# Kernel optimization log

Hardware: AMD Instinct MI355X
Metric: run time of the kernel (lower is better)

The kernel has to match this reference:

```python
import jax, jax.numpy as jnp
import numpy as np

WINDOW_SIZE = 11
SIGMA = 1.5
WEIGHTS = np.array([0.0448, 0.2856, 0.3001, 0.2363, 0.1333], dtype=np.float32)
LEVELS = 5


def _gaussian(ws, sigma):
    x = np.arange(ws, dtype=np.float32)
    g = np.exp(-((x - ws // 2) ** 2) / (2.0 * sigma ** 2))
    return g / g.sum()


def _window3d(ws, channel):
    g = _gaussian(ws, SIGMA)
    w3 = np.einsum('i,j,k->ijk', g, g, g).astype(np.float32)  # [ws,ws,ws]
    # OIDHW, depthwise: O=channel, I=1
    return jnp.asarray(np.broadcast_to(w3[None, None], (channel, 1, ws, ws, ws)))


def _conv3d(x, w, channel):
    return jax.lax.conv_general_dilated(
        x, w, window_strides=(1, 1, 1), padding='VALID',
        dimension_numbers=('NCDHW', 'OIDHW', 'NCDHW'),
        feature_group_count=channel)


def _avg_pool3d(x):
    s = jax.lax.reduce_window(x, 0.0, jax.lax.add,
                              (1, 1, 2, 2, 2), (1, 1, 2, 2, 2), 'VALID')
    return s / 8.0


def _ssim(img1, img2, window_size):
    _, channel, d, h, w = img1.shape
    # val_range=None branch: L derived from img1 statistics
    max_val = jnp.where(jnp.max(img1) > 128, 255.0, 1.0)
    min_val = jnp.where(jnp.min(img1) < -0.5, -1.0, 0.0)
    L = max_val - min_val
    real_size = min(window_size, d, h, w)
    win = _window3d(real_size, channel)

    mu1 = _conv3d(img1, win, channel)
    mu2 = _conv3d(img2, win, channel)
    mu1_sq = mu1 * mu1
    mu2_sq = mu2 * mu2
    mu1_mu2 = mu1 * mu2
    sigma1_sq = _conv3d(img1 * img1, win, channel) - mu1_sq
    sigma2_sq = _conv3d(img2 * img2, win, channel) - mu2_sq
    sigma12 = _conv3d(img1 * img2, win, channel) - mu1_mu2

    C1 = (0.01 * L) ** 2
    C2 = (0.03 * L) ** 2
    v1 = 2.0 * sigma12 + C2
    v2 = sigma1_sq + sigma2_sq + C2
    cs = jnp.mean(v1 / v2)
    ssim_map = (2.0 * mu1_mu2 + C1) * v1 / ((mu1_sq + mu2_sq + C1) * v2)
    return jnp.mean(ssim_map), cs


def setup_inputs() -> dict:
    key = jax.random.key(0)
    k1, k2 = jax.random.split(key)
    shape = (2, 1, 192, 192, 192)
    img1 = jax.random.normal(k1, shape, dtype=jnp.float32)
    img2 = jax.random.normal(k2, shape, dtype=jnp.float32)
    return {"img1": img1, "img2": img2}


def reference(img1, img2):
    weights = jnp.asarray(WEIGHTS)
    ssims, mcs = [], []
    for _ in range(LEVELS):
        sim, cs = _ssim(img1, img2, WINDOW_SIZE)
        ssims.append(sim)
        mcs.append(cs)
        img1 = _avg_pool3d(img1)
        img2 = _avg_pool3d(img2)
    ssims = jnp.stack(ssims)
    mcs = jnp.stack(mcs)
    pow1 = mcs ** weights
    pow2 = ssims ** weights
    return jnp.prod(pow1[:-1]) * pow2[-1]
```

## Files before the change

### kernel.cpp

```cpp
#include <hip/hip_runtime.h>
#include <math.h>


__device__ __forceinline__ unsigned enc_f(float f) {
    unsigned u = __float_as_uint(f);
    return (u & 0x80000000u) ? ~u : (u | 0x80000000u);
}
__device__ __forceinline__ float dec_f(unsigned e) {
    unsigned u = (e & 0x80000000u) ? (e ^ 0x80000000u) : ~e;
    return __uint_as_float(u);
}

__global__ void init_kernel(float* wsf) {
    unsigned* wsu = (unsigned*)wsf;
    int t = threadIdx.x;
    if (t < 10)       wsf[t] = 0.0f;
    else if (t < 15)  wsu[t] = 0xFFFFFFFFu;
    else if (t < 20)  wsu[t] = 0u;
    else if (t == 20) wsu[t] = 0u;
}

struct PyrParams {
    const float* src[2];
    float* dst[2][4];
};

__launch_bounds__(256, 4)
__global__ void pyramid_kernel(PyrParams P, float* wsf) {
    __shared__ float L1[16 * 256];
    __shared__ float L2[512];
    __shared__ float L3[64];
    __shared__ float smn[4], smx[4];
    unsigned* wsu = (unsigned*)wsf;

    const int tid = threadIdx.x;
    int blk = blockIdx.x;
    int r = blk % 216; blk /= 216;
    int batch = blk & 1;
    int im = blk >> 1;
    const int rx = r % 6, ry = (r / 6) % 6, rz = r / 36;

    const long N0 = 192L * 192 * 192;
    const float* src = P.src[im] + (long)batch * N0;
    float* d1 = P.dst[im][0] + (long)batch * 96 * 96 * 96;
    float* d2 = P.dst[im][1] + (long)batch * 48 * 48 * 48;
    float* d3 = P.dst[im][2] + (long)batch * 24 * 24 * 24;
    float* d4 = P.dst[im][3] + (long)batch * 12 * 12 * 12;

    const int tx = tid & 15, ty = tid >> 4;
    float mnv[5], mxv[5];
#pragma unroll
    for (int l = 0; l < 5; l++) { mnv[l] = INFINITY; mxv[l] = -INFINITY; }

    const long D = 192, D2 = 192L * 192;
    const int gx = 2 * (rx * 16 + tx);
    const int gy = 2 * (ry * 16 + ty);
#pragma unroll 4
    for (int z = 0; z < 16; z++) {
        const int gz = 2 * (rz * 16 + z);
        long base = (long)gz * D2 + (long)gy * D + gx;
        float2 a00 = *(const float2*)(src + base);
        float2 a01 = *(const float2*)(src + base + D);
        float2 a10 = *(const float2*)(src + base + D2);
        float2 a11 = *(const float2*)(src + base + D2 + D);
        float lo = fminf(fminf(fminf(a00.x, a00.y), fminf(a01.x, a01.y)),
                         fminf(fminf(a10.x, a10.y), fminf(a11.x, a11.y)));
        float hi = fmaxf(fmaxf(fmaxf(a00.x, a00.y), fmaxf(a01.x, a01.y)),
                         fmaxf(fmaxf(a10.x, a10.y), fmaxf(a11.x, a11.y)));
        mnv[0] = fminf(mnv[0], lo); mxv[0] = fmaxf(mxv[0], hi);
        float s = (a00.x + a00.y + a01.x + a01.y +
                   a10.x + a10.y + a11.x + a11.y) * 0.125f;
        mnv[1] = fminf(mnv[1], s); mxv[1] = fmaxf(mxv[1], s);
        d1[(long)(rz * 16 + z) * 96 * 96 + (ry * 16 + ty) * 96 + (rx * 16 + tx)] = s;
        L1[z * 256 + ty * 16 + tx] = s;
    }
    __syncthreads();

#pragma unroll
    for (int k = 0; k < 2; k++) {
        int o = tid + (k << 8);
        int x = o & 7, y = (o >> 3) & 7, z = o >> 6;
        float s = (L1[(2 * z) * 256 + (2 * y) * 16 + 2 * x] +
                   L1[(2 * z) * 256 + (2 * y) * 16 + 2 * x + 1] +
                   L1[(2 * z) * 256 + (2 * y + 1) * 16 + 2 * x] +
                   L1[(2 * z) * 256 + (2 * y + 1) * 16 + 2 * x + 1] +
                   L1[(2 * z + 1) * 256 + (2 * y) * 16 + 2 * x] +
                   L1[(2 * z + 1) * 256 + (2 * y) * 16 + 2 * x + 1] +
                   L1[(2 * z + 1) * 256 + (2 * y + 1) * 16 + 2 * x] +
                   L1[(2 * z + 1) * 256 + (2 * y + 1) * 16 + 2 * x + 1]) * 0.125f;
        mnv[2] = fminf(mnv[2], s); mxv[2] = fmaxf(mxv[2], s);
        d2[(long)(rz * 8 + z) * 48 * 48 + (ry * 8 + y) * 48 + (rx * 8 + x)] = s;
        L2[o] = s;
    }
    __syncthreads();

    if (tid < 64) {
        int x = tid & 3, y = (tid >> 2) & 3, z = tid >> 4;
        float s = (L2[(2 * z) * 64 + (2 * y) * 8 + 2 * x] +
                   L2[(2 * z) * 64 + (2 * y) * 8 + 2 * x + 1] +
                   L2[(2 * z) * 64 + (2 * y + 1) * 8 + 2 * x] +
                   L2[(2 * z) * 64 + (2 * y + 1) * 8 + 2 * x + 1] +
                   L2[(2 * z + 1) * 64 + (2 * y) * 8 + 2 * x] +
                   L2[(2 * z + 1) * 64 + (2 * y) * 8 + 2 * x + 1] +
                   L2[(2 * z + 1) * 64 + (2 * y + 1) * 8 + 2 * x] +
                   L2[(2 * z + 1) * 64 + (2 * y + 1) * 8 + 2 * x + 1]) * 0.125f;
        mnv[3] = fminf(mnv[3], s); mxv[3] = fmaxf(mxv[3], s);
        d3[(long)(rz * 4 + z) * 24 * 24 + (ry * 4 + y) * 24 + (rx * 4 + x)] = s;
        L3[tid] = s;
    }
    __syncthreads();

    if (tid < 8) {
        int x = tid & 1, y = (tid >> 1) & 1, z = tid >> 2;
        float s = (L3[(2 * z) * 16 + (2 * y) * 4 + 2 * x] +
                   L3[(2 * z) * 16 + (2 * y) * 4 + 2 * x + 1] +
                   L3[(2 * z) * 16 + (2 * y + 1) * 4 + 2 * x] +
                   L3[(2 * z) * 16 + (2 * y + 1) * 4 + 2 * x + 1] +
                   L3[(2 * z + 1) * 16 + (2 * y) * 4 + 2 * x] +
                   L3[(2 * z + 1) * 16 + (2 * y) * 4 + 2 * x + 1] +
                   L3[(2 * z + 1) * 16 + (2 * y + 1) * 4 + 2 * x] +
                   L3[(2 * z + 1) * 16 + (2 * y + 1) * 4 + 2 * x + 1]) * 0.125f;
        mnv[4] = fminf(mnv[4], s); mxv[4] = fmaxf(mxv[4], s);
        d4[(long)(rz * 2 + z) * 12 * 12 + (ry * 2 + y) * 12 + (rx * 2 + x)] = s;
    }

    const int lane = tid & 63, w = tid >> 6;
#pragma unroll
    for (int l = 0; l < 5; l++) {
        float mn = mnv[l], mx = mxv[l];
        for (int o = 32; o; o >>= 1) {
            mn = fminf(mn, __shfl_down(mn, o));
            mx = fmaxf(mx, __shfl_down(mx, o));
        }
        __syncthreads();
        if (lane == 0) { smn[w] = mn; smx[w] = mx; }
        __syncthreads();
        if (tid == 0 && im == 0) {
            for (int i = 1; i < 4; i++) { mn = fminf(mn, smn[i]); mx = fmaxf(mx, smx[i]); }
            atomicMin(&wsu[10 + l], enc_f(mn));
            atomicMax(&wsu[15 + l], enc_f(mx));
        }
    }
}

#define TSX 16
#define TSY 32
#define EXR 42
#define EXC 26
#define SPS 30
#define NPIX (EXR * EXC)
#define TPS 17

struct AllParams {
    const float* A[5];
    const float* B[5];
    int D[5], O[5], zc[5], nTx[5], nTy[5];
    int blk0[6];
    float* out;
    double cnt[5];
};

__launch_bounds__(256, 2)
__attribute__((amdgpu_waves_per_eu(2, 2)))
__global__ void ssim_all_kernel(AllParams P, float* wsf) {
    __shared__ __align__(16) float2 S[EXR * SPS];
    __shared__ __align__(16) float4 TX4[EXR * TPS];
    __shared__ float TXe[EXR * TPS];
    __shared__ float2 RED[256];

    const int tid = threadIdx.x;
    const int col = tid & 15;
    const int yg  = tid >> 4;

    int level = 0;
    {
        int b = blockIdx.x;
#pragma unroll
        for (int l = 1; l < 5; l++)
            if (b >= P.blk0[l]) level = l;
    }
    int rel = blockIdx.x - P.blk0[level];
    const int D   = P.D[level];
    const int O   = P.O[level];
    const int ZC  = P.zc[level];
    const int nTx = P.nTx[level];
    const int nTy = P.nTy[level];

    const int tx = rel % nTx;  rel /= nTx;
    const int ty = rel % nTy;  rel /= nTy;
    const int batch = rel & 1;
    const int chunk = rel >> 1;

    const int oz0 = chunk * ZC;
    const int oz1 = min(oz0 + ZC, O);
    const int nplanes = oz1 - oz0 + 10;
    const int ox0 = tx * TSX;
    const int oy0 = ty * TSY;
    const int D2  = D * D;
    const float* A = P.A[level] + (long)batch * D * D2;
    const float* B = P.B[level] + (long)batch * D * D2;

    float g[11];
    {
        float s = 0.f;
#pragma unroll
        for (int i = 0; i < 11; i++) {
            float d = (float)(i - 5);
            g[i] = expf(-d * d / 4.5f);
            s += g[i];
        }
#pragma unroll
        for (int i = 0; i < 11; i++) g[i] /= s;
    }

    const unsigned* wsu = (const unsigned*)wsf;
    float mxv = dec_f(wsu[15 + level]);
    float mnv = dec_f(wsu[10 + level]);
    float maxval = (mxv > 128.f) ? 255.f : 1.f;
    float minval = (mnv < -0.5f) ? -1.f : 0.f;
    float Lr = maxval - minval;
    float C1 = 0.01f * Lr; C1 *= C1;
    float C2 = 0.03f * Lr; C2 *= C2;

    int  poff[5], sidx[5];
    bool pval[5];
#pragma unroll
    for (int k = 0; k < 5; k++) {
        int idx = tid + (k << 8);
        pval[k] = (idx < NPIX);
        int row = idx / EXC;
        int c   = idx - row * EXC;
        sidx[k] = row * SPS + c;
        int gy = min(oy0 + row, D - 1);
        int gx = min(ox0 + c,   D - 1);
        poff[k] = gy * D + gx;
    }

    float Acc[10][11] = {};
    float ssim_acc = 0.f, cs_acc = 0.f;

    const bool vx  = (ox0 + col < O);
    const bool vy0 = vx && (oy0 + 2 * yg < O);
    const bool vy1 = vx && (oy0 + 2 * yg + 1 < O);

    float2 Pld[5];
    {
        long zoff = (long)oz0 * D2;
#pragma unroll
        for (int k = 0; k < 5; k++)
            if (pval[k]) Pld[k] = make_float2(A[zoff + poff[k]], B[zoff + poff[k]]);
    }

    for (int pc = 0; pc < nplanes; ++pc) {
        __syncthreads();
#pragma unroll
        for (int k = 0; k < 5; k++)
            if (pval[k]) S[sidx[k]] = Pld[k];
        if (pc + 1 < nplanes) {
            long zoff = (long)(oz0 + pc + 1) * D2;
#pragma unroll
            for (int k = 0; k < 5; k++)
                if (pval[k]) Pld[k] = make_float2(A[zoff + poff[k]], B[zoff + poff[k]]);
        }
        __syncthreads();

        if (tid < EXR * 4) {
            int row = tid >> 2;
            int cg  = tid & 3;
            const float4* srow = (const float4*)(S + row * SPS);
            float pa[14], pb[14];
#pragma unroll
            for (int i = 0; i < 7; i++) {
                float4 q = srow[2 * cg + i];
                pa[2 * i] = q.x; pb[2 * i] = q.y;
                pa[2 * i + 1] = q.z; pb[2 * i + 1] = q.w;
            }
#pragma unroll
            for (int cc = 0; cc < 4; cc++) {
                float m1 = 0.f, m2 = 0.f, aa = 0.f, bb = 0.f, ab = 0.f;
#pragma unroll
                for (int j = 0; j < 11; j++) {
                    float w = g[j];
                    float a = pa[cc + j], b = pb[cc + j];
                    float wa = w * a, wb = w * b;
                    m1 += wa; m2 += wb;
                    aa += wa * a; bb += wb * b; ab += wa * b;
                }
                int o = row * TPS + 4 * cg + cc;
                TX4[o] = make_float4(m1, m2, aa, bb);
                TXe[o] = ab;
            }
        }
        __syncthreads();

        float se[5] = {0.f, 0.f, 0.f, 0.f, 0.f};
        float so[5] = {0.f, 0.f, 0.f, 0.f, 0.f};
#pragma unroll
        for (int j = 0; j < 12; j++) {
            int o = (2 * yg + j) * TPS + col;
            float4 q = TX4[o];
            float e  = TXe[o];
            if (j < 11) {
                float w = g[j];
                se[0] += w * q.x; se[1] += w * q.y; se[2] += w * q.z;
                se[3] += w * q.w; se[4] += w * e;
            }
            if (j > 0) {
                float w = g[j - 1];
                so[0] += w * q.x; so[1] += w * q.y; so[2] += w * q.z;
                so[3] += w * q.w; so[4] += w * e;
            }
        }

#pragma unroll
        for (int f = 0; f < 5; f++) {
#pragma unroll
            for (int k = 0; k < 10; k++)
                Acc[2 * f][k] = fmaf(g[10 - k], se[f], Acc[2 * f][k + 1]);
            Acc[2 * f][10] = g[0] * se[f];
#pragma unroll
            for (int k = 0; k < 10; k++)
                Acc[2 * f + 1][k] = fmaf(g[10 - k], so[f], Acc[2 * f + 1][k + 1]);
            Acc[2 * f + 1][10] = g[0] * so[f];
        }

        if (pc >= 10) {
#pragma unroll
            for (int r = 0; r < 2; r++) {
                bool valid = r ? vy1 : vy0;
                if (!valid) continue;
                float m1  = Acc[0 + r][0], m2  = Acc[2 + r][0];
                float s11 = Acc[4 + r][0], s22 = Acc[6 + r][0], s12 = Acc[8 + r][0];
                float mu11 = m1 * m1, mu22 = m2 * m2, mu12 = m1 * m2;
                float sg1 = s11 - mu11, sg2 = s22 - mu22, sg12 = s12 - mu12;
                float v1 = 2.f * sg12 + C2;
                float v2 = sg1 + sg2 + C2;
                cs_acc   += v1 / v2;
                ssim_acc += ((2.f * mu12 + C1) * v1) / ((mu11 + mu22 + C1) * v2);
            }
        }
    }

    RED[tid] = make_float2(ssim_acc, cs_acc);
    __syncthreads();
    for (int s = 128; s > 0; s >>= 1) {
        if (tid < s) {
            RED[tid].x += RED[tid + s].x;
            RED[tid].y += RED[tid + s].y;
        }
        __syncthreads();
    }
    if (tid == 0) {
        atomicAdd(&wsf[level],     RED[0].x);
        atomicAdd(&wsf[5 + level], RED[0].y);
        __threadfence();
        unsigned prev = atomicAdd((unsigned*)wsf + 20, 1u);
        if (prev == (unsigned)(P.blk0[5] - 1)) {
            double w[5];
            w[0] = (double)0.0448f; w[1] = (double)0.2856f; w[2] = (double)0.3001f;
            w[3] = (double)0.2363f; w[4] = (double)0.1333f;
            double prod = 1.0;
            for (int l = 0; l < 4; l++) {
                float cs = atomicAdd(&wsf[5 + l], 0.0f);
                prod *= pow((double)cs / P.cnt[l], w[l]);
            }
            float sm = atomicAdd(&wsf[4], 0.0f);
            prod *= pow((double)sm / P.cnt[4], w[4]);
            P.out[0] = (float)prod;
        }
    }
}

extern "C" void kernel_launch(void* const* d_in, const int* in_sizes, int n_in,
                              void* d_out, int out_size, void* d_ws, size_t ws_size,
                              hipStream_t stream) {
    (void)in_sizes; (void)n_in; (void)out_size; (void)ws_size;
    const float* img1 = (const float*)d_in[0];
    const float* img2 = (const float*)d_in[1];
    float* wsf = (float*)d_ws;
    float* out = (float*)d_out;

    const int Ds[5]  = {192, 96, 48, 24, 12};
    const int ZCs[5] = {26, 16, 14, 14, 2};

    float* bufA[5] = {nullptr};
    float* bufB[5] = {nullptr};
    size_t o = 32;
    for (int l = 1; l < 5; l++) {
        long n = 2L * Ds[l] * Ds[l] * Ds[l];
        bufA[l] = wsf + o; o += (size_t)n;
        bufB[l] = wsf + o; o += (size_t)n;
    }

    init_kernel<<<1, 64, 0, stream>>>(wsf);

    PyrParams PP;
    PP.src[0] = img1; PP.src[1] = img2;
    for (int l = 1; l < 5; l++) { PP.dst[0][l - 1] = bufA[l]; PP.dst[1][l - 1] = bufB[l]; }
    pyramid_kernel<<<216 * 2 * 2, 256, 0, stream>>>(PP, wsf);

    AllParams P;
    P.A[0] = img1; P.B[0] = img2;
    for (int l = 1; l < 5; l++) { P.A[l] = bufA[l]; P.B[l] = bufB[l]; }
    P.out = out;
    int acc = 0;
    for (int l = 0; l < 5; l++) {
        int D = Ds[l], O = D - 10, ZC = ZCs[l];
        int nTx = (O + TSX - 1) / TSX;
        int nTy = (O + TSY - 1) / TSY;
        int ZCn = (O + ZC - 1) / ZC;
        P.D[l] = D; P.O[l] = O; P.zc[l] = ZC; P.nTx[l] = nTx; P.nTy[l] = nTy;
        P.blk0[l] = acc;
        acc += nTx * nTy * 2 * ZCn;
        double Od = (double)O;
        P.cnt[l] = 2.0 * Od * Od * Od;
    }
    P.blk0[5] = acc;
    ssim_all_kernel<<<acc, 256, 0, stream>>>(P, wsf);
}
```

Before: 358.6 us.

## Fuse init, pyramid and SSIM into one persistent cooperative kernel

```diff
diff --git a/kernel.cpp b/kernel.cpp
--- a/kernel.cpp
+++ b/kernel.cpp
@@ -1,5 +1,8 @@
 #include <hip/hip_runtime.h>
+#include <hip/hip_cooperative_groups.h>
 #include <math.h>
+
+namespace cg = cooperative_groups;
 
 
 __device__ __forceinline__ unsigned enc_f(float f) {
@@ -11,138 +14,6 @@
     return __uint_as_float(u);
 }
 
-__global__ void init_kernel(float* wsf) {
-    unsigned* wsu = (unsigned*)wsf;
-    int t = threadIdx.x;
-    if (t < 10)       wsf[t] = 0.0f;
-    else if (t < 15)  wsu[t] = 0xFFFFFFFFu;
-    else if (t < 20)  wsu[t] = 0u;
-    else if (t == 20) wsu[t] = 0u;
-}
-
-struct PyrParams {
-    const float* src[2];
-    float* dst[2][4];
-};
-
-__launch_bounds__(256, 4)
-__global__ void pyramid_kernel(PyrParams P, float* wsf) {
-    __shared__ float L1[16 * 256];
-    __shared__ float L2[512];
-    __shared__ float L3[64];
-    __shared__ float smn[4], smx[4];
-    unsigned* wsu = (unsigned*)wsf;
-
-    const int tid = threadIdx.x;
-    int blk = blockIdx.x;
-    int r = blk % 216; blk /= 216;
-    int batch = blk & 1;
-    int im = blk >> 1;
-    const int rx = r % 6, ry = (r / 6) % 6, rz = r / 36;
-
-    const long N0 = 192L * 192 * 192;
-    const float* src = P.src[im] + (long)batch * N0;
-    float* d1 = P.dst[im][0] + (long)batch * 96 * 96 * 96;
-    float* d2 = P.dst[im][1] + (long)batch * 48 * 48 * 48;
-    float* d3 = P.dst[im][2] + (long)batch * 24 * 24 * 24;
-    float* d4 = P.dst[im][3] + (long)batch * 12 * 12 * 12;
-
-    const int tx = tid & 15, ty = tid >> 4;
-    float mnv[5], mxv[5];
-#pragma unroll
-    for (int l = 0; l < 5; l++) { mnv[l] = INFINITY; mxv[l] = -INFINITY; }
-
-    const long D = 192, D2 = 192L * 192;
-    const int gx = 2 * (rx * 16 + tx);
-    const int gy = 2 * (ry * 16 + ty);
-#pragma unroll 4
-    for (int z = 0; z < 16; z++) {
-        const int gz = 2 * (rz * 16 + z);
-        long base = (long)gz * D2 + (long)gy * D + gx;
-        float2 a00 = *(const float2*)(src + base);
-        float2 a01 = *(const float2*)(src + base + D);
-        float2 a10 = *(const float2*)(src + base + D2);
-        float2 a11 = *(const float2*)(src + base + D2 + D);
-        float lo = fminf(fminf(fminf(a00.x, a00.y), fminf(a01.x, a01.y)),
-                         fminf(fminf(a10.x, a10.y), fminf(a11.x, a11.y)));
-        float hi = fmaxf(fmaxf(fmaxf(a00.x, a00.y), fmaxf(a01.x, a01.y)),
-                         fmaxf(fmaxf(a10.x, a10.y), fmaxf(a11.x, a11.y)));
-        mnv[0] = fminf(mnv[0], lo); mxv[0] = fmaxf(mxv[0], hi);
-        float s = (a00.x + a00.y + a01.x + a01.y +
-                   a10.x + a10.y + a11.x + a11.y) * 0.125f;
-        mnv[1] = fminf(mnv[1], s); mxv[1] = fmaxf(mxv[1], s);
-        d1[(long)(rz * 16 + z) * 96 * 96 + (ry * 16 + ty) * 96 + (rx * 16 + tx)] = s;
-        L1[z * 256 + ty * 16 + tx] = s;
-    }
-    __syncthreads();
-
-#pragma unroll
-    for (int k = 0; k < 2; k++) {
-        int o = tid + (k << 8);
-        int x = o & 7, y = (o >> 3) & 7, z = o >> 6;
-        float s = (L1[(2 * z) * 256 + (2 * y) * 16 + 2 * x] +
-                   L1[(2 * z) * 256 + (2 * y) * 16 + 2 * x + 1] +
-                   L1[(2 * z) * 256 + (2 * y + 1) * 16 + 2 * x] +
-                   L1[(2 * z) * 256 + (2 * y + 1) * 16 + 2 * x + 1] +
-                   L1[(2 * z + 1) * 256 + (2 * y) * 16 + 2 * x] +
-                   L1[(2 * z + 1) * 256 + (2 * y) * 16 + 2 * x + 1] +
-                   L1[(2 * z + 1) * 256 + (2 * y + 1) * 16 + 2 * x] +
-                   L1[(2 * z + 1) * 256 + (2 * y + 1) * 16 + 2 * x + 1]) * 0.125f;
-        mnv[2] = fminf(mnv[2], s); mxv[2] = fmaxf(mxv[2], s);
-        d2[(long)(rz * 8 + z) * 48 * 48 + (ry * 8 + y) * 48 + (rx * 8 + x)] = s;
-        L2[o] = s;
-    }
-    __syncthreads();
-
-    if (tid < 64) {
-        int x = tid & 3, y = (tid >> 2) & 3, z = tid >> 4;
-        float s = (L2[(2 * z) * 64 + (2 * y) * 8 + 2 * x] +
-                   L2[(2 * z) * 64 + (2 * y) * 8 + 2 * x + 1] +
-                   L2[(2 * z) * 64 + (2 * y + 1) * 8 + 2 * x] +
-                   L2[(2 * z) * 64 + (2 * y + 1) * 8 + 2 * x + 1] +
-                   L2[(2 * z + 1) * 64 + (2 * y) * 8 + 2 * x] +
-                   L2[(2 * z + 1) * 64 + (2 * y) * 8 + 2 * x + 1] +
-                   L2[(2 * z + 1) * 64 + (2 * y + 1) * 8 + 2 * x] +
-                   L2[(2 * z + 1) * 64 + (2 * y + 1) * 8 + 2 * x + 1]) * 0.125f;
-        mnv[3] = fminf(mnv[3], s); mxv[3] = fmaxf(mxv[3], s);
-        d3[(long)(rz * 4 + z) * 24 * 24 + (ry * 4 + y) * 24 + (rx * 4 + x)] = s;
-        L3[tid] = s;
-    }
-    __syncthreads();
-
-    if (tid < 8) {
-        int x = tid & 1, y = (tid >> 1) & 1, z = tid >> 2;
-        float s = (L3[(2 * z) * 16 + (2 * y) * 4 + 2 * x] +
-                   L3[(2 * z) * 16 + (2 * y) * 4 + 2 * x + 1] +
-                   L3[(2 * z) * 16 + (2 * y + 1) * 4 + 2 * x] +
-                   L3[(2 * z) * 16 + (2 * y + 1) * 4 + 2 * x + 1] +
-                   L3[(2 * z + 1) * 16 + (2 * y) * 4 + 2 * x] +
-                   L3[(2 * z + 1) * 16 + (2 * y) * 4 + 2 * x + 1] +
-                   L3[(2 * z + 1) * 16 + (2 * y + 1) * 4 + 2 * x] +
-                   L3[(2 * z + 1) * 16 + (2 * y + 1) * 4 + 2 * x + 1]) * 0.125f;
-        mnv[4] = fminf(mnv[4], s); mxv[4] = fmaxf(mxv[4], s);
-        d4[(long)(rz * 2 + z) * 12 * 12 + (ry * 2 + y) * 12 + (rx * 2 + x)] = s;
-    }
-
-    const int lane = tid & 63, w = tid >> 6;
-#pragma unroll
-    for (int l = 0; l < 5; l++) {
-        float mn = mnv[l], mx = mxv[l];
-        for (int o = 32; o; o >>= 1) {
-            mn = fminf(mn, __shfl_down(mn, o));
-            mx = fmaxf(mx, __shfl_down(mx, o));
-        }
-        __syncthreads();
-        if (lane == 0) { smn[w] = mn; smx[w] = mx; }
-        __syncthreads();
-        if (tid == 0 && im == 0) {
-            for (int i = 1; i < 4; i++) { mn = fminf(mn, smn[i]); mx = fmaxf(mx, smx[i]); }
-            atomicMin(&wsu[10 + l], enc_f(mn));
-            atomicMax(&wsu[15 + l], enc_f(mx));
-        }
-    }
-}
-
 #define TSX 16
 #define TSY 32
 #define EXR 42
@@ -151,7 +22,9 @@
 #define NPIX (EXR * EXC)
 #define TPS 17
 
-struct AllParams {
+struct MegaParams {
+    const float* src[2];
+    float* dst[2][4];
     const float* A[5];
     const float* B[5];
     int D[5], O[5], zc[5], nTx[5], nTy[5];
@@ -160,45 +33,151 @@
     double cnt[5];
 };
 
+#define LDS_BYTES 26912
+
 __launch_bounds__(256, 2)
 __attribute__((amdgpu_waves_per_eu(2, 2)))
-__global__ void ssim_all_kernel(AllParams P, float* wsf) {
-    __shared__ __align__(16) float2 S[EXR * SPS];
-    __shared__ __align__(16) float4 TX4[EXR * TPS];
-    __shared__ float TXe[EXR * TPS];
-    __shared__ float2 RED[256];
-
+__global__ void mega_kernel(MegaParams P, float* wsf) {
+    __shared__ __align__(16) char LB[LDS_BYTES];
+    __shared__ int sItem;
+    unsigned* wsu = (unsigned*)wsf;
     const int tid = threadIdx.x;
+
+    if (blockIdx.x == 0) {
+        if (tid < 10)       wsf[tid] = 0.0f;
+        else if (tid < 15)  wsu[tid] = 0xFFFFFFFFu;
+        else if (tid < 20)  wsu[tid] = 0u;
+        else if (tid < 22)  wsu[tid] = 0u;
+    }
+    cg::this_grid().sync();
+
+    {
+        float* L1  = (float*)LB;
+        float* L2s = (float*)(LB + 16384);
+        float* L3s = (float*)(LB + 18432);
+        float* smn = (float*)(LB + 18688);
+        float* smx = (float*)(LB + 18704);
+
+        for (int p = blockIdx.x; p < 864; p += gridDim.x) {
+            int blk = p;
+            int r = blk % 216; blk /= 216;
+            int batch = blk & 1;
+            int im = blk >> 1;
+            const int rx = r % 6, ry = (r / 6) % 6, rz = r / 36;
+
+            const long N0 = 192L * 192 * 192;
+            const float* src = P.src[im] + (long)batch * N0;
+            float* d1 = P.dst[im][0] + (long)batch * 96 * 96 * 96;
+            float* d2 = P.dst[im][1] + (long)batch * 48 * 48 * 48;
+            float* d3 = P.dst[im][2] + (long)batch * 24 * 24 * 24;
+            float* d4 = P.dst[im][3] + (long)batch * 12 * 12 * 12;
+
+            const int tx = tid & 15, ty = tid >> 4;
+            float mnv[5], mxv[5];
+#pragma unroll
+            for (int l = 0; l < 5; l++) { mnv[l] = INFINITY; mxv[l] = -INFINITY; }
+
+            const long D = 192, D2 = 192L * 192;
+            const int gx = 2 * (rx * 16 + tx);
+            const int gy = 2 * (ry * 16 + ty);
+#pragma unroll 4
+            for (int z = 0; z < 16; z++) {
+                const int gz = 2 * (rz * 16 + z);
+                long base = (long)gz * D2 + (long)gy * D + gx;
+                float2 a00 = *(const float2*)(src + base);
+                float2 a01 = *(const float2*)(src + base + D);
+                float2 a10 = *(const float2*)(src + base + D2);
+                float2 a11 = *(const float2*)(src + base + D2 + D);
+                float lo = fminf(fminf(fminf(a00.x, a00.y), fminf(a01.x, a01.y)),
+                                 fminf(fminf(a10.x, a10.y), fminf(a11.x, a11.y)));
+                float hi = fmaxf(fmaxf(fmaxf(a00.x, a00.y), fmaxf(a01.x, a01.y)),
+                                 fmaxf(fmaxf(a10.x, a10.y), fmaxf(a11.x, a11.y)));
+                mnv[0] = fminf(mnv[0], lo); mxv[0] = fmaxf(mxv[0], hi);
+                float s = (a00.x + a00.y + a01.x + a01.y +
+                           a10.x + a10.y + a11.x + a11.y) * 0.125f;
+                mnv[1] = fminf(mnv[1], s); mxv[1] = fmaxf(mxv[1], s);
+                d1[(long)(rz * 16 + z) * 96 * 96 + (ry * 16 + ty) * 96 + (rx * 16 + tx)] = s;
+                L1[z * 256 + ty * 16 + tx] = s;
+            }
+            __syncthreads();
+
+#pragma unroll
+            for (int k = 0; k < 2; k++) {
+                int o = tid + (k << 8);
+                int x = o & 7, y = (o >> 3) & 7, z = o >> 6;
+                float s = (L1[(2 * z) * 256 + (2 * y) * 16 + 2 * x] +
+                           L1[(2 * z) * 256 + (2 * y) * 16 + 2 * x + 1] +
+                           L1[(2 * z) * 256 + (2 * y + 1) * 16 + 2 * x] +
+                           L1[(2 * z) * 256 + (2 * y + 1) * 16 + 2 * x + 1] +
+                           L1[(2 * z + 1) * 256 + (2 * y) * 16 + 2 * x] +
+                           L1[(2 * z + 1) * 256 + (2 * y) * 16 + 2 * x + 1] +
+                           L1[(2 * z + 1) * 256 + (2 * y + 1) * 16 + 2 * x] +
+                           L1[(2 * z + 1) * 256 + (2 * y + 1) * 16 + 2 * x + 1]) * 0.125f;
+                mnv[2] = fminf(mnv[2], s); mxv[2] = fmaxf(mxv[2], s);
+                d2[(long)(rz * 8 + z) * 48 * 48 + (ry * 8 + y) * 48 + (rx * 8 + x)] = s;
+                L2s[o] = s;
+            }
+            __syncthreads();
+
+            if (tid < 64) {
+                int x = tid & 3, y = (tid >> 2) & 3, z = tid >> 4;
+                float s = (L2s[(2 * z) * 64 + (2 * y) * 8 + 2 * x] +
+                           L2s[(2 * z) * 64 + (2 * y) * 8 + 2 * x + 1] +
+                           L2s[(2 * z) * 64 + (2 * y + 1) * 8 + 2 * x] +
+                           L2s[(2 * z) * 64 + (2 * y + 1) * 8 + 2 * x + 1] +
+                           L2s[(2 * z + 1) * 64 + (2 * y) * 8 + 2 * x] +
+                           L2s[(2 * z + 1) * 64 + (2 * y) * 8 + 2 * x + 1] +
+                           L2s[(2 * z + 1) * 64 + (2 * y + 1) * 8 + 2 * x] +
+                           L2s[(2 * z + 1) * 64 + (2 * y + 1) * 8 + 2 * x + 1]) * 0.125f;
+                mnv[3] = fminf(mnv[3], s); mxv[3] = fmaxf(mxv[3], s);
+                d3[(long)(rz * 4 + z) * 24 * 24 + (ry * 4 + y) * 24 + (rx * 4 + x)] = s;
+                L3s[tid] = s;
+            }
+            __syncthreads();
+
+            if (tid < 8) {
+                int x = tid & 1, y = (tid >> 1) & 1, z = tid >> 2;
+                float s = (L3s[(2 * z) * 16 + (2 * y) * 4 + 2 * x] +
+                           L3s[(2 * z) * 16 + (2 * y) * 4 + 2 * x + 1] +
+                           L3s[(2 * z) * 16 + (2 * y + 1) * 4 + 2 * x] +
+                           L3s[(2 * z) * 16 + (2 * y + 1) * 4 + 2 * x + 1] +
+                           L3s[(2 * z + 1) * 16 + (2 * y) * 4 + 2 * x] +
+                           L3s[(2 * z + 1) * 16 + (2 * y) * 4 + 2 * x + 1] +
+                           L3s[(2 * z + 1) * 16 + (2 * y + 1) * 4 + 2 * x] +
+                           L3s[(2 * z + 1) * 16 + (2 * y + 1) * 4 + 2 * x + 1]) * 0.125f;
+                mnv[4] = fminf(mnv[4], s); mxv[4] = fmaxf(mxv[4], s);
+                d4[(long)(rz * 2 + z) * 12 * 12 + (ry * 2 + y) * 12 + (rx * 2 + x)] = s;
+            }
+
+            const int lane = tid & 63, w = tid >> 6;
+#pragma unroll
+            for (int l = 0; l < 5; l++) {
+                float mn = mnv[l], mx = mxv[l];
+                for (int o = 32; o; o >>= 1) {
+                    mn = fminf(mn, __shfl_down(mn, o));
+                    mx = fmaxf(mx, __shfl_down(mx, o));
+                }
+                __syncthreads();
+                if (lane == 0) { smn[w] = mn; smx[w] = mx; }
+                __syncthreads();
+                if (tid == 0 && im == 0) {
+                    for (int i = 1; i < 4; i++) { mn = fminf(mn, smn[i]); mx = fmaxf(mx, smx[i]); }
+                    atomicMin(&wsu[10 + l], enc_f(mn));
+                    atomicMax(&wsu[15 + l], enc_f(mx));
+                }
+            }
+            __syncthreads();
+        }
+    }
+    cg::this_grid().sync();
+
+    float2* S   = (float2*)LB;
+    float4* TX4 = (float4*)(LB + 10080);
+    float*  TXe = (float*)(LB + 21504);
+    float2* RED = (float2*)(LB + 24360);
+
     const int col = tid & 15;
     const int yg  = tid >> 4;
-
-    int level = 0;
-    {
-        int b = blockIdx.x;
-#pragma unroll
-        for (int l = 1; l < 5; l++)
-            if (b >= P.blk0[l]) level = l;
-    }
-    int rel = blockIdx.x - P.blk0[level];
-    const int D   = P.D[level];
-    const int O   = P.O[level];
-    const int ZC  = P.zc[level];
-    const int nTx = P.nTx[level];
-    const int nTy = P.nTy[level];
-
-    const int tx = rel % nTx;  rel /= nTx;
-    const int ty = rel % nTy;  rel /= nTy;
-    const int batch = rel & 1;
-    const int chunk = rel >> 1;
-
-    const int oz0 = chunk * ZC;
-    const int oz1 = min(oz0 + ZC, O);
-    const int nplanes = oz1 - oz0 + 10;
-    const int ox0 = tx * TSX;
-    const int oy0 = ty * TSY;
-    const int D2  = D * D;
-    const float* A = P.A[level] + (long)batch * D * D2;
-    const float* B = P.B[level] + (long)batch * D * D2;
 
     float g[11];
     {
@@ -213,160 +192,193 @@
         for (int i = 0; i < 11; i++) g[i] /= s;
     }
 
-    const unsigned* wsu = (const unsigned*)wsf;
-    float mxv = dec_f(wsu[15 + level]);
-    float mnv = dec_f(wsu[10 + level]);
-    float maxval = (mxv > 128.f) ? 255.f : 1.f;
-    float minval = (mnv < -0.5f) ? -1.f : 0.f;
-    float Lr = maxval - minval;
-    float C1 = 0.01f * Lr; C1 *= C1;
-    float C2 = 0.03f * Lr; C2 *= C2;
-
-    int  poff[5], sidx[5];
-    bool pval[5];
-#pragma unroll
-    for (int k = 0; k < 5; k++) {
-        int idx = tid + (k << 8);
-        pval[k] = (idx < NPIX);
-        int row = idx / EXC;
-        int c   = idx - row * EXC;
-        sidx[k] = row * SPS + c;
-        int gy = min(oy0 + row, D - 1);
-        int gx = min(ox0 + c,   D - 1);
-        poff[k] = gy * D + gx;
-    }
-
-    float Acc[10][11] = {};
-    float ssim_acc = 0.f, cs_acc = 0.f;
-
-    const bool vx  = (ox0 + col < O);
-    const bool vy0 = vx && (oy0 + 2 * yg < O);
-    const bool vy1 = vx && (oy0 + 2 * yg + 1 < O);
-
-    float2 Pld[5];
-    {
-        long zoff = (long)oz0 * D2;
-#pragma unroll
-        for (int k = 0; k < 5; k++)
-            if (pval[k]) Pld[k] = make_float2(A[zoff + poff[k]], B[zoff + poff[k]]);
-    }
-
-    for (int pc = 0; pc < nplanes; ++pc) {
+    const int nItems = P.blk0[5];
+
+    for (;;) {
+        if (tid == 0) sItem = (int)atomicAdd(&wsu[21], 1u);
         __syncthreads();
-#pragma unroll
-        for (int k = 0; k < 5; k++)
-            if (pval[k]) S[sidx[k]] = Pld[k];
-        if (pc + 1 < nplanes) {
-            long zoff = (long)(oz0 + pc + 1) * D2;
+        const int item = sItem;
+        if (item >= nItems) break;
+
+        int level = 0;
+#pragma unroll
+        for (int l = 1; l < 5; l++)
+            if (item >= P.blk0[l]) level = l;
+        int rel = item - P.blk0[level];
+        const int D   = P.D[level];
+        const int O   = P.O[level];
+        const int ZC  = P.zc[level];
+        const int nTx = P.nTx[level];
+        const int nTy = P.nTy[level];
+
+        const int tx = rel % nTx;  rel /= nTx;
+        const int ty = rel % nTy;  rel /= nTy;
+        const int batch = rel & 1;
+        const int chunk = rel >> 1;
+
+        const int oz0 = chunk * ZC;
+        const int oz1 = min(oz0 + ZC, O);
+        const int nplanes = oz1 - oz0 + 10;
+        const int ox0 = tx * TSX;
+        const int oy0 = ty * TSY;
+        const int D2  = D * D;
+        const float* A = P.A[level] + (long)batch * D * D2;
+        const float* B = P.B[level] + (long)batch * D * D2;
+
+        float mxv = dec_f(wsu[15 + level]);
+        float mnv = dec_f(wsu[10 + level]);
+        float maxval = (mxv > 128.f) ? 255.f : 1.f;
+        float minval = (mnv < -0.5f) ? -1.f : 0.f;
+        float Lr = maxval - minval;
+        float C1 = 0.01f * Lr; C1 *= C1;
+        float C2 = 0.03f * Lr; C2 *= C2;
+
+        int  poff[5], sidx[5];
+        bool pval[5];
+#pragma unroll
+        for (int k = 0; k < 5; k++) {
+            int idx = tid + (k << 8);
+            pval[k] = (idx < NPIX);
+            int row = idx / EXC;
+            int c   = idx - row * EXC;
+            sidx[k] = row * SPS + c;
+            int gyy = min(oy0 + row, D - 1);
+            int gxx = min(ox0 + c,   D - 1);
+            poff[k] = gyy * D + gxx;
+        }
+
+        float Acc[10][11] = {};
+        float ssim_acc = 0.f, cs_acc = 0.f;
+
+        const bool vx  = (ox0 + col < O);
+        const bool vy0 = vx && (oy0 + 2 * yg < O);
+        const bool vy1 = vx && (oy0 + 2 * yg + 1 < O);
+
+        float2 Pld[5];
+        {
+            long zoff = (long)oz0 * D2;
 #pragma unroll
             for (int k = 0; k < 5; k++)
                 if (pval[k]) Pld[k] = make_float2(A[zoff + poff[k]], B[zoff + poff[k]]);
         }
+
+        for (int pc = 0; pc < nplanes; ++pc) {
+            __syncthreads();
+#pragma unroll
+            for (int k = 0; k < 5; k++)
+                if (pval[k]) S[sidx[k]] = Pld[k];
+            if (pc + 1 < nplanes) {
+                long zoff = (long)(oz0 + pc + 1) * D2;
+#pragma unroll
+                for (int k = 0; k < 5; k++)
+                    if (pval[k]) Pld[k] = make_float2(A[zoff + poff[k]], B[zoff + poff[k]]);
+            }
+            __syncthreads();
+
+            if (tid < EXR * 4) {
+                int row = tid >> 2;
+                int cg2 = tid & 3;
+                const float4* srow = (const float4*)(S + row * SPS);
+                float pa[14], pb[14];
+#pragma unroll
+                for (int i = 0; i < 7; i++) {
+                    float4 q = srow[2 * cg2 + i];
+                    pa[2 * i] = q.x; pb[2 * i] = q.y;
+                    pa[2 * i + 1] = q.z; pb[2 * i + 1] = q.w;
+                }
+#pragma unroll
+                for (int cc = 0; cc < 4; cc++) {
+                    float m1 = 0.f, m2 = 0.f, aa = 0.f, bb = 0.f, ab = 0.f;
+#pragma unroll
+                    for (int j = 0; j < 11; j++) {
+                        float w = g[j];
+                        float a = pa[cc + j], b = pb[cc + j];
+                        float wa = w * a, wb = w * b;
+                        m1 += wa; m2 += wb;
+                        aa += wa * a; bb += wb * b; ab += wa * b;
+                    }
+                    int o = row * TPS + 4 * cg2 + cc;
+                    TX4[o] = make_float4(m1, m2, aa, bb);
+                    TXe[o] = ab;
+                }
+            }
+            __syncthreads();
+
+            float se[5] = {0.f, 0.f, 0.f, 0.f, 0.f};
+            float so[5] = {0.f, 0.f, 0.f, 0.f, 0.f};
+#pragma unroll
+            for (int j = 0; j < 12; j++) {
+                int o = (2 * yg + j) * TPS + col;
+                float4 q = TX4[o];
+                float e  = TXe[o];
+                if (j < 11) {
+                    float w = g[j];
+                    se[0] += w * q.x; se[1] += w * q.y; se[2] += w * q.z;
+                    se[3] += w * q.w; se[4] += w * e;
+                }
+                if (j > 0) {
+                    float w = g[j - 1];
+                    so[0] += w * q.x; so[1] += w * q.y; so[2] += w * q.z;
+                    so[3] += w * q.w; so[4] += w * e;
+                }
+            }
+
+#pragma unroll
+            for (int f = 0; f < 5; f++) {
+#pragma unroll
+                for (int k = 0; k < 10; k++)
+                    Acc[2 * f][k] = fmaf(g[10 - k], se[f], Acc[2 * f][k + 1]);
+                Acc[2 * f][10] = g[0] * se[f];
+#pragma unroll
+                for (int k = 0; k < 10; k++)
+                    Acc[2 * f + 1][k] = fmaf(g[10 - k], so[f], Acc[2 * f + 1][k + 1]);
+                Acc[2 * f + 1][10] = g[0] * so[f];
+            }
+
+            if (pc >= 10) {
+#pragma unroll
+                for (int rr = 0; rr < 2; rr++) {
+                    bool valid = rr ? vy1 : vy0;
+                    if (!valid) continue;
+                    float m1  = Acc[0 + rr][0], m2  = Acc[2 + rr][0];
+                    float s11 = Acc[4 + rr][0], s22 = Acc[6 + rr][0], s12 = Acc[8 + rr][0];
+                    float mu11 = m1 * m1, mu22 = m2 * m2, mu12 = m1 * m2;
+                    float sg1 = s11 - mu11, sg2 = s22 - mu22, sg12 = s12 - mu12;
+                    float v1 = 2.f * sg12 + C2;
+                    float v2 = sg1 + sg2 + C2;
+                    cs_acc   += v1 / v2;
+                    ssim_acc += ((2.f * mu12 + C1) * v1) / ((mu11 + mu22 + C1) * v2);
+                }
+            }
+        }
+
+        RED[tid] = make_float2(ssim_acc, cs_acc);
         __syncthreads();
-
-        if (tid < EXR * 4) {
-            int row = tid >> 2;
-            int cg  = tid & 3;
-            const float4* srow = (const float4*)(S + row * SPS);
-            float pa[14], pb[14];
-#pragma unroll
-            for (int i = 0; i < 7; i++) {
-                float4 q = srow[2 * cg + i];
-                pa[2 * i] = q.x; pb[2 * i] = q.y;
-                pa[2 * i + 1] = q.z; pb[2 * i + 1] = q.w;
-            }
-#pragma unroll
-            for (int cc = 0; cc < 4; cc++) {
-                float m1 = 0.f, m2 = 0.f, aa = 0.f, bb = 0.f, ab = 0.f;
-#pragma unroll
-                for (int j = 0; j < 11; j++) {
-                    float w = g[j];
-                    float a = pa[cc + j], b = pb[cc + j];
-                    float wa = w * a, wb = w * b;
-                    m1 += wa; m2 += wb;
-                    aa += wa * a; bb += wb * b; ab += wa * b;
-                }
-                int o = row * TPS + 4 * cg + cc;
-                TX4[o] = make_float4(m1, m2, aa, bb);
-                TXe[o] = ab;
-            }
-        }
-        __syncthreads();
-
-        float se[5] = {0.f, 0.f, 0.f, 0.f, 0.f};
-        float so[5] = {0.f, 0.f, 0.f, 0.f, 0.f};
-#pragma unroll
-        for (int j = 0; j < 12; j++) {
-            int o = (2 * yg + j) * TPS + col;
-            float4 q = TX4[o];
-            float e  = TXe[o];
-            if (j < 11) {
-                float w = g[j];
-                se[0] += w * q.x; se[1] += w * q.y; se[2] += w * q.z;
-                se[3] += w * q.w; se[4] += w * e;
-            }
-            if (j > 0) {
-                float w = g[j - 1];
-                so[0] += w * q.x; so[1] += w * q.y; so[2] += w * q.z;
-                so[3] += w * q.w; so[4] += w * e;
-            }
-        }
-
-#pragma unroll
-        for (int f = 0; f < 5; f++) {
-#pragma unroll
-            for (int k = 0; k < 10; k++)
-                Acc[2 * f][k] = fmaf(g[10 - k], se[f], Acc[2 * f][k + 1]);
-            Acc[2 * f][10] = g[0] * se[f];
-#pragma unroll
-            for (int k = 0; k < 10; k++)
-                Acc[2 * f + 1][k] = fmaf(g[10 - k], so[f], Acc[2 * f + 1][k + 1]);
-            Acc[2 * f + 1][10] = g[0] * so[f];
-        }
-
-        if (pc >= 10) {
-#pragma unroll
-            for (int r = 0; r < 2; r++) {
-                bool valid = r ? vy1 : vy0;
-                if (!valid) continue;
-                float m1  = Acc[0 + r][0], m2  = Acc[2 + r][0];
-                float s11 = Acc[4 + r][0], s22 = Acc[6 + r][0], s12 = Acc[8 + r][0];
-                float mu11 = m1 * m1, mu22 = m2 * m2, mu12 = m1 * m2;
-                float sg1 = s11 - mu11, sg2 = s22 - mu22, sg12 = s12 - mu12;
-                float v1 = 2.f * sg12 + C2;
-                float v2 = sg1 + sg2 + C2;
-                cs_acc   += v1 / v2;
-                ssim_acc += ((2.f * mu12 + C1) * v1) / ((mu11 + mu22 + C1) * v2);
-            }
-        }
-    }
-
-    RED[tid] = make_float2(ssim_acc, cs_acc);
-    __syncthreads();
-    for (int s = 128; s > 0; s >>= 1) {
-        if (tid < s) {
-            RED[tid].x += RED[tid + s].x;
-            RED[tid].y += RED[tid + s].y;
-        }
-        __syncthreads();
-    }
-    if (tid == 0) {
-        atomicAdd(&wsf[level],     RED[0].x);
-        atomicAdd(&wsf[5 + level], RED[0].y);
-        __threadfence();
-        unsigned prev = atomicAdd((unsigned*)wsf + 20, 1u);
-        if (prev == (unsigned)(P.blk0[5] - 1)) {
-            double w[5];
-            w[0] = (double)0.0448f; w[1] = (double)0.2856f; w[2] = (double)0.3001f;
-            w[3] = (double)0.2363f; w[4] = (double)0.1333f;
-            double prod = 1.0;
-            for (int l = 0; l < 4; l++) {
-                float cs = atomicAdd(&wsf[5 + l], 0.0f);
-                prod *= pow((double)cs / P.cnt[l], w[l]);
-            }
-            float sm = atomicAdd(&wsf[4], 0.0f);
-            prod *= pow((double)sm / P.cnt[4], w[4]);
-            P.out[0] = (float)prod;
+        for (int s = 128; s > 0; s >>= 1) {
+            if (tid < s) {
+                RED[tid].x += RED[tid + s].x;
+                RED[tid].y += RED[tid + s].y;
+            }
+            __syncthreads();
+        }
+        if (tid == 0) {
+            atomicAdd(&wsf[level],     RED[0].x);
+            atomicAdd(&wsf[5 + level], RED[0].y);
+            __threadfence();
+            unsigned prev = atomicAdd(&wsu[20], 1u);
+            if (prev == (unsigned)(nItems - 1)) {
+                double w[5];
+                w[0] = (double)0.0448f; w[1] = (double)0.2856f; w[2] = (double)0.3001f;
+                w[3] = (double)0.2363f; w[4] = (double)0.1333f;
+                double prod = 1.0;
+                for (int l = 0; l < 4; l++) {
+                    float cs = atomicAdd(&wsf[5 + l], 0.0f);
+                    prod *= pow((double)cs / P.cnt[l], w[l]);
+                }
+                float sm = atomicAdd(&wsf[4], 0.0f);
+                prod *= pow((double)sm / P.cnt[4], w[4]);
+                P.out[0] = (float)prod;
+            }
         }
     }
 }
@@ -392,14 +404,9 @@
         bufB[l] = wsf + o; o += (size_t)n;
     }
 
-    init_kernel<<<1, 64, 0, stream>>>(wsf);
-
-    PyrParams PP;
-    PP.src[0] = img1; PP.src[1] = img2;
-    for (int l = 1; l < 5; l++) { PP.dst[0][l - 1] = bufA[l]; PP.dst[1][l - 1] = bufB[l]; }
-    pyramid_kernel<<<216 * 2 * 2, 256, 0, stream>>>(PP, wsf);
-
-    AllParams P;
+    MegaParams P;
+    P.src[0] = img1; P.src[1] = img2;
+    for (int l = 1; l < 5; l++) { P.dst[0][l - 1] = bufA[l]; P.dst[1][l - 1] = bufB[l]; }
     P.A[0] = img1; P.B[0] = img2;
     for (int l = 1; l < 5; l++) { P.A[l] = bufA[l]; P.B[l] = bufB[l]; }
     P.out = out;
@@ -416,5 +423,14 @@
         P.cnt[l] = 2.0 * Od * Od * Od;
     }
     P.blk0[5] = acc;
-    ssim_all_kernel<<<acc, 256, 0, stream>>>(P, wsf);
+
+    int nb = 0;
+    hipOccupancyMaxActiveBlocksPerMultiprocessor(&nb, mega_kernel, 256, 0);
+    if (nb < 1) nb = 1;
+    int G = nb * 256;
+    if (G > 512) G = 512;
+
+    void* args[] = {(void*)&P, (void*)&wsf};
+    hipLaunchCooperativeKernel((const void*)mega_kernel, dim3(G), dim3(256),
+                               args, 0, stream);
 }
```

Result: slower. 536.4 us (+49.6%).
